# Performance work log

Hardware: AMD Instinct MI355X
Metric: run time of the kernel (lower is better)

The kernel has to match this reference:

```python
import jax, jax.numpy as jnp
import numpy as np

B, N, D, H = 4, 4096, 1024, 16
DH = D // H            # 64
GH = 4 * DH            # gate hidden = 256
FREQ = N // 2 + 1      # 2049
INV_SQRT2 = 0.7071067811865476


def _ln(x, g, b, eps=1e-6):
    mu = jnp.mean(x, axis=-1, keepdims=True)
    var = jnp.mean((x - mu) ** 2, axis=-1, keepdims=True)
    return (x - mu) / jnp.sqrt(var + eps) * g + b


def _xavier(k, out_f, in_f, gain=0.8):
    bound = gain * (6.0 / (in_f + out_f)) ** 0.5
    return jax.random.uniform(k, (out_f, in_f), jnp.float32, -bound, bound)


def setup_inputs() -> dict:
    key = jax.random.key(0)
    ks = jax.random.split(key, 8)
    return {
        'x': jax.random.normal(ks[0], (B, N, D), jnp.float32),
        'Wq': _xavier(ks[1], D, D),
        'Wv': _xavier(ks[2], D, D),
        'Wo': _xavier(ks[3], D, D),
        'ln_g': jnp.ones((DH,), jnp.float32),
        'ln_b': jnp.zeros((DH,), jnp.float32),
        'Wgup': _xavier(ks[4], GH, DH),
        'Wgdn': _xavier(ks[5], 2 * FREQ, GH),
        'Wwup': _xavier(ks[6], GH, DH),
        'Wwdn': _xavier(ks[7], N, GH),
    }


def reference(x, Wq, Wv, Wo, ln_g, ln_b, Wgup, Wgdn, Wwup, Wwdn):
    Bx, Nx, Dx = x.shape
    # projections -> [B, H, N, DH]
    q = (x @ Wq.T).reshape(Bx, Nx, H, DH).transpose(0, 2, 1, 3)
    v = (x @ Wv.T).reshape(Bx, Nx, H, DH).transpose(0, 2, 1, 3)
    # per-head summary token -> complex spectral gate over FREQ bins
    bar = _ln(q.mean(axis=2), ln_g, ln_b)                    # [B, H, DH]
    gr = (jax.nn.silu(bar @ Wgup.T) @ Wgdn.T)               # [B, H, 2*FREQ]
    gr = gr.reshape(Bx, H, FREQ, 2)
    gate = jax.lax.complex(gr[..., 0], gr[..., 1])           # [B, H, FREQ]
    # spectral mixing (chunk == seq_len, power-of-two path)
    spec = jnp.fft.rfft(v, axis=2, norm='ortho') * gate[..., None]
    v_t = jnp.fft.irfft(spec, n=Nx, axis=2, norm='ortho')    # [B, H, N, DH]
    # Haar wavelet refinement
    even, odd = v_t[..., ::2, :], v_t[..., 1::2, :]
    w = jnp.concatenate([even + odd, even - odd], axis=-2) * INV_SQRT2
    s = (jax.nn.silu(bar @ Wwup.T) @ Wwdn.T)[..., None]      # [B, H, N, 1]
    w = w * s
    half = Nx // 2
    low, high = w[..., :half, :], w[..., half:, :]
    # interleave even/odd back along seq dim
    refine = jnp.stack([low + high, low - high], axis=-2).reshape(Bx, H, Nx, DH) * INV_SQRT2
    v_t = v_t + refine
    y = v_t.transpose(0, 2, 1, 3).reshape(Bx, Nx, Dx)
    return y @ Wo.T
```

## Files before the change

kernel.cpp:

```cpp
#include <hip/hip_runtime.h>

constexpr int CB = 4, CN = 4096, CD = 1024, CH = 16, CDH = 64, CGH = 256, CFREQ = 2049, CBH = 64;

constexpr size_t OFF_XSUM = 0;
constexpr size_t OFF_HG   = 4096;
constexpr size_t OFF_HW   = OFF_HG + (size_t)CBH * CGH;
constexpr size_t OFF_GATE = OFF_HW + (size_t)CBH * CGH;
constexpr size_t OFF_S    = OFF_GATE + (size_t)CBH * 2 * CFREQ;
constexpr size_t OFF_CA   = OFF_S + (size_t)CBH * CN;
constexpr size_t OFF_CD   = OFF_CA + (size_t)CBH * (CN / 2);
constexpr size_t OFF_TW   = OFF_CD + (size_t)CBH * (CN / 2);
constexpr size_t OFF_VCOL = OFF_TW + 8192;
constexpr size_t OFF_XHI  = OFF_VCOL + (size_t)CB * CD * CN;
constexpr size_t OFF_XLO  = OFF_XHI + (size_t)CB * CN * CD / 2;
constexpr size_t OFF_WVHI = OFF_XLO + (size_t)CB * CN * CD / 2;
constexpr size_t OFF_WVLO = OFF_WVHI + (size_t)CD * CD / 2;
constexpr size_t OFF_WOHI = OFF_WVLO + (size_t)CD * CD / 2;
constexpr size_t OFF_WOLO = OFF_WOHI + (size_t)CD * CD / 2;

typedef __bf16 bf16x8 __attribute__((ext_vector_type(8)));
typedef __bf16 bf16x4 __attribute__((ext_vector_type(4)));
typedef float  f32x4  __attribute__((ext_vector_type(4)));
typedef float  f32x16 __attribute__((ext_vector_type(16)));

__device__ __forceinline__ float silu_f(float x) { return x / (1.0f + expf(-x)); }

__device__ __forceinline__ void gload16(const void* g, void* l) {
    __builtin_amdgcn_global_load_lds(
        reinterpret_cast<const __attribute__((address_space(1))) unsigned int*>(
            reinterpret_cast<uintptr_t>(g)),
        reinterpret_cast<__attribute__((address_space(3))) unsigned int*>(
            reinterpret_cast<uintptr_t>(l)),
        16, 0, 0);
}

__device__ __forceinline__ float2 cadd(float2 a, float2 b) { return make_float2(a.x + b.x, a.y + b.y); }
__device__ __forceinline__ float2 csub(float2 a, float2 b) { return make_float2(a.x - b.x, a.y - b.y); }
__device__ __forceinline__ float2 cmul(float2 a, float2 b) { return make_float2(a.x * b.x - a.y * b.y, a.x * b.y + a.y * b.x); }
__device__ __forceinline__ float2 cmulc(float2 a, float2 b) { return make_float2(a.x * b.x + a.y * b.y, a.y * b.x - a.x * b.y); }
__device__ __forceinline__ float2 mulni(float2 a) { return make_float2(a.y, -a.x); }
__device__ __forceinline__ float2 mulpi(float2 a) { return make_float2(-a.y, a.x); }

__device__ __forceinline__ int P(int r) { return r + (r >> 3); }

__device__ __forceinline__ int drev8(int k) {
    return ((k & 7) << 9) | (((k >> 3) & 7) << 6) | (((k >> 6) & 7) << 3) | ((k >> 9) & 7);
}

__device__ __forceinline__ void dft8_fwd(const float2 a[8], float2 A[8]) {
    float2 t0 = cadd(a[0], a[4]), t1 = csub(a[0], a[4]);
    float2 t2 = cadd(a[2], a[6]), t3 = mulni(csub(a[2], a[6]));
    float2 t4 = cadd(a[1], a[5]), t5 = csub(a[1], a[5]);
    float2 t6 = cadd(a[3], a[7]), t7 = mulni(csub(a[3], a[7]));
    float2 u0 = cadd(t0, t2), u1 = csub(t0, t2);
    float2 u2 = cadd(t1, t3), u3 = csub(t1, t3);
    float2 u4 = cadd(t4, t6), u5 = mulni(csub(t4, t6));
    float2 u6 = cadd(t5, t7), u7 = csub(t5, t7);
    const float s = 0.70710678118654752f;
    float2 w6 = make_float2(s * (u6.x + u6.y), s * (u6.y - u6.x));
    float2 w7 = make_float2(s * (u7.y - u7.x), -s * (u7.x + u7.y));
    A[0] = cadd(u0, u4); A[4] = csub(u0, u4);
    A[2] = cadd(u1, u5); A[6] = csub(u1, u5);
    A[1] = cadd(u2, w6); A[5] = csub(u2, w6);
    A[3] = cadd(u3, w7); A[7] = csub(u3, w7);
}

__device__ __forceinline__ void dft8_inv(const float2 a[8], float2 A[8]) {
    float2 t0 = cadd(a[0], a[4]), t1 = csub(a[0], a[4]);
    float2 t2 = cadd(a[2], a[6]), t3 = mulpi(csub(a[2], a[6]));
    float2 t4 = cadd(a[1], a[5]), t5 = csub(a[1], a[5]);
    float2 t6 = cadd(a[3], a[7]), t7 = mulpi(csub(a[3], a[7]));
    float2 u0 = cadd(t0, t2), u1 = csub(t0, t2);
    float2 u2 = cadd(t1, t3), u3 = csub(t1, t3);
    float2 u4 = cadd(t4, t6), u5 = mulpi(csub(t4, t6));
    float2 u6 = cadd(t5, t7), u7 = csub(t5, t7);
    const float s = 0.70710678118654752f;
    float2 w6 = make_float2(s * (u6.x - u6.y), s * (u6.x + u6.y));
    float2 w7 = make_float2(-s * (u7.x + u7.y), s * (u7.x - u7.y));
    A[0] = cadd(u0, u4); A[4] = csub(u0, u4);
    A[2] = cadd(u1, u5); A[6] = csub(u1, u5);
    A[1] = cadd(u2, w6); A[5] = csub(u2, w6);
    A[3] = cadd(u3, w7); A[7] = csub(u3, w7);
}

template <int M>
__device__ __forceinline__ void fwd_stage(float2* buf, const float2* __restrict__ tw, int t) {
    int j = t & (M - 1);
    int i0 = ((t & ~(M - 1)) << 3) + j;
    constexpr int TS = 512 / M;
    float2 a[8], A[8];
#pragma unroll
    for (int c = 0; c < 8; ++c) a[c] = buf[P(i0 + c * M)];
    dft8_fwd(a, A);
#pragma unroll
    for (int p = 0; p < 8; ++p) {
        float2 v = (M > 1 && p) ? cmul(A[p], tw[j * p * TS]) : A[p];
        buf[P(i0 + p * M)] = v;
    }
}

template <int M>
__device__ __forceinline__ void inv_stage(float2* buf, const float2* __restrict__ tw, int t) {
    int j = t & (M - 1);
    int i0 = ((t & ~(M - 1)) << 3) + j;
    constexpr int TS = 512 / M;
    float2 a[8], A[8];
#pragma unroll
    for (int c = 0; c < 8; ++c) {
        float2 v = buf[P(i0 + c * M)];
        a[c] = (M > 1 && c) ? cmulc(v, tw[j * c * TS]) : v;
    }
    dft8_inv(a, A);
#pragma unroll
    for (int p = 0; p < 8; ++p) buf[P(i0 + p * M)] = A[p];
}

__global__ void k_tw(float* twf) {
    int i = blockIdx.x * 256 + threadIdx.x;
    if (i < 4096) {
        double ang = -2.0 * 3.14159265358979323846 * (double)i / 4096.0;
        twf[2 * i]     = (float)cos(ang);
        twf[2 * i + 1] = (float)sin(ang);
    }
}

__global__ __launch_bounds__(256) void k_meansplit(const float* __restrict__ X, float* __restrict__ xsum,
                                                   __bf16* __restrict__ hi, __bf16* __restrict__ lo) {
    int b = blockIdx.y;
    int c = blockIdx.x;
    int t = threadIdx.x;
    int half = t >> 7;
    int col = (t & 127) * 8;
    size_t base = (size_t)b * CN * CD + ((size_t)c * 64 + half * 32) * CD + col;
    float acc[8];
#pragma unroll
    for (int j = 0; j < 8; ++j) acc[j] = 0.f;
    for (int n = 0; n < 32; ++n) {
        size_t o = base + (size_t)n * CD;
        float4 v0 = *(const float4*)(X + o);
        float4 v1 = *(const float4*)(X + o + 4);
        float vv[8] = {v0.x, v0.y, v0.z, v0.w, v1.x, v1.y, v1.z, v1.w};
        bf16x8 hv, lv;
#pragma unroll
        for (int j = 0; j < 8; ++j) {
            acc[j] += vv[j];
            __bf16 h = (__bf16)vv[j];
            hv[j] = h;
            lv[j] = (__bf16)(vv[j] - (float)h);
        }
        *(bf16x8*)&hi[o] = hv;
        *(bf16x8*)&lo[o] = lv;
    }
#pragma unroll
    for (int j = 0; j < 8; ++j) atomicAdd(&xsum[b * CD + col + j], acc[j]);
}

__global__ __launch_bounds__(256) void k_barhidden(const float* __restrict__ xsum,
                                                   const float* __restrict__ Wq,
                                                   const float* __restrict__ ln_g,
                                                   const float* __restrict__ ln_b,
                                                   const float* __restrict__ Wgup,
                                                   const float* __restrict__ Wwup,
                                                   float* __restrict__ hg, float* __restrict__ hw) {
    int bh = blockIdx.x;
    int b = bh >> 4, h = bh & 15;
    int t = threadIdx.x;
    __shared__ float part[256];
    __shared__ float bar_s[64];
    int dh = t >> 2, seg = t & 3;
    const float* wrow = Wq + (size_t)(h * 64 + dh) * CD + seg * 256;
    const float* xs = xsum + b * CD + seg * 256;
    float acc = 0.f;
    for (int i = 0; i < 256; i += 4) {
        float4 w4 = *(const float4*)(wrow + i);
        float4 x4 = *(const float4*)(xs + i);
        acc += w4.x * x4.x + w4.y * x4.y + w4.z * x4.z + w4.w * x4.w;
    }
    part[t] = acc;
    __syncthreads();
    if (t < 64) {
        float q = (part[4 * t] + part[4 * t + 1] + part[4 * t + 2] + part[4 * t + 3]) * (1.0f / 4096.0f);
        float mu = q;
        for (int o = 32; o >= 1; o >>= 1) mu += __shfl_xor(mu, o, 64);
        mu *= (1.0f / 64.0f);
        float dev = q - mu;
        float vv = dev * dev;
        for (int o = 32; o >= 1; o >>= 1) vv += __shfl_xor(vv, o, 64);
        vv *= (1.0f / 64.0f);
        bar_s[t] = dev / sqrtf(vv + 1e-6f) * ln_g[t] + ln_b[t];
    }
    __syncthreads();
    const float* gup = Wgup + (size_t)t * CDH;
    const float* wup = Wwup + (size_t)t * CDH;
    float ag = 0.f, aw = 0.f;
    for (int i = 0; i < CDH; i += 4) {
        float4 bb = *(const float4*)(&bar_s[i]);
        float4 g4 = *(const float4*)(gup + i);
        float4 w4 = *(const float4*)(wup + i);
        ag += g4.x * bb.x + g4.y * bb.y + g4.z * bb.z + g4.w * bb.w;
        aw += w4.x * bb.x + w4.y * bb.y + w4.z * bb.z + w4.w * bb.w;
    }
    hg[bh * CGH + t] = silu_f(ag);
    hw[bh * CGH + t] = silu_f(aw);
}

__global__ __launch_bounds__(256) void k_gategemv(const float* __restrict__ Wgdn,
                                                  const float* __restrict__ Wwdn,
                                                  const float* __restrict__ hg,
                                                  const float* __restrict__ hw,
                                                  float* __restrict__ gate, float* __restrict__ sbuf) {
    int z = blockIdx.z;
    const float* Wd = z ? Wwdn : Wgdn;
    const float* hid = z ? hw : hg;
    float* out = z ? sbuf : gate;
    int Kout = z ? CN : 2 * CFREQ;
    int bh0 = blockIdx.y * 8;
    int t = threadIdx.x;
    int k = blockIdx.x * 256 + t;
    __shared__ float Lh[8][256];
    for (int g = 0; g < 8; ++g) Lh[g][t] = hid[(size_t)(bh0 + g) * CGH + t];
    __syncthreads();
    if (k >= Kout) return;
    float accv[8] = {0.f, 0.f, 0.f, 0.f, 0.f, 0.f, 0.f, 0.f};
    const float* wrow = Wd + (size_t)k * CGH;
    for (int j4 = 0; j4 < 64; ++j4) {
        float4 wv = *(const float4*)(wrow + 4 * j4);
#pragma unroll
        for (int g = 0; g < 8; ++g) {
            accv[g] += wv.x * Lh[g][4 * j4] + wv.y * Lh[g][4 * j4 + 1] +
                       wv.z * Lh[g][4 * j4 + 2] + wv.w * Lh[g][4 * j4 + 3];
        }
    }
    for (int g = 0; g < 8; ++g) out[(size_t)(bh0 + g) * Kout + k] = accv[g];
}

__global__ __launch_bounds__(256) void k_coef(const float* __restrict__ sbuf,
                                              float* __restrict__ ca, float* __restrict__ cd) {
    int bh = blockIdx.y;
    int i = blockIdx.x * 256 + threadIdx.x;
    float s0 = sbuf[(size_t)bh * CN + i];
    float s1 = sbuf[(size_t)bh * CN + 2048 + i];
    ca[(size_t)bh * 2048 + i] = 1.0f + 0.5f * (s0 + s1);
    cd[(size_t)bh * 2048 + i] = 0.5f * (s0 - s1);
}

__global__ __launch_bounds__(256) void k_split(const float* __restrict__ src,
                                               __bf16* __restrict__ hi, __bf16* __restrict__ lo,
                                               int n4) {
    int i = blockIdx.x * 256 + threadIdx.x;
    int stride = gridDim.x * 256;
    for (; i < n4; i += stride) {
        float4 v = ((const float4*)src)[i];
        __bf16 h0 = (__bf16)v.x, h1 = (__bf16)v.y, h2 = (__bf16)v.z, h3 = (__bf16)v.w;
        bf16x4 hv = {h0, h1, h2, h3};
        bf16x4 lv = {(__bf16)(v.x - (float)h0), (__bf16)(v.y - (float)h1),
                     (__bf16)(v.z - (float)h2), (__bf16)(v.w - (float)h3)};
        *(bf16x4*)&hi[4 * (size_t)i] = hv;
        *(bf16x4*)&lo[4 * (size_t)i] = lv;
    }
}

__global__ __launch_bounds__(256) void k_tsplit(const float* __restrict__ Vcol,
                                                __bf16* __restrict__ hi, __bf16* __restrict__ lo) {
    __shared__ float tile[32][33];
    int bx = blockIdx.x;
    int by = blockIdx.y;
    int b  = blockIdx.z;
    int t = threadIdx.x;
    int d = t >> 3, n4 = (t & 7) * 4;
    const float* src = Vcol + ((size_t)b * CD + by * 32 + d) * CN + bx * 32 + n4;
    float4 v = *(const float4*)src;
    tile[d][n4] = v.x; tile[d][n4 + 1] = v.y; tile[d][n4 + 2] = v.z; tile[d][n4 + 3] = v.w;
    __syncthreads();
    int n = t >> 3, d4 = (t & 7) * 4;
    size_t o = ((size_t)b * CN + bx * 32 + n) * CD + by * 32 + d4;
    float x0 = tile[d4][n], x1 = tile[d4 + 1][n], x2 = tile[d4 + 2][n], x3 = tile[d4 + 3][n];
    __bf16 h0 = (__bf16)x0, h1 = (__bf16)x1, h2 = (__bf16)x2, h3 = (__bf16)x3;
    bf16x4 hv = {h0, h1, h2, h3};
    bf16x4 lv = {(__bf16)(x0 - (float)h0), (__bf16)(x1 - (float)h1),
                 (__bf16)(x2 - (float)h2), (__bf16)(x3 - (float)h3)};
    *(bf16x4*)&hi[o] = hv;
    *(bf16x4*)&lo[o] = lv;
}

template <int TRANS>
__global__ __launch_bounds__(512, 2) void k_mfma_gemm(const __bf16* __restrict__ Ahi,
                                                      const __bf16* __restrict__ Alo,
                                                      const __bf16* __restrict__ Bhi,
                                                      const __bf16* __restrict__ Blo,
                                                      float* __restrict__ C) {
    __shared__ __align__(16) __bf16 lds[2][4][256 * 32];
    int t = threadIdx.x;
    int l = t & 63, w = t >> 6;
    int wm = w >> 2, wn = w & 3;
    int hw = blockIdx.x;
    int xcd = hw & 7, slot = hw >> 3;
    int m0 = (xcd * 8 + (slot >> 2)) * 256;
    int n0 = (slot & 3) * 256;

    int pl = w >> 1;
    const __bf16* gsrc = (pl == 0) ? Ahi : (pl == 1) ? Alo : (pl == 2) ? Bhi : Blo;
    int gr0 = (pl < 2) ? m0 : n0;
    unsigned o[8];
    int rl0[8];
#pragma unroll
    for (int i = 0; i < 8; ++i) {
        int rl = (w & 1) * 128 + i * 16 + (l >> 2);
        unsigned sq = (unsigned)((l & 3) ^ ((rl >> 2) & 3));
        o[i] = (unsigned)(gr0 + rl) * 1024u + sq * 8u;
        rl0[i] = (w & 1) * 128 + i * 16;
    }

    f32x16 acc[4][2];
#pragma unroll
    for (int mi = 0; mi < 4; ++mi)
#pragma unroll
        for (int ni = 0; ni < 2; ++ni)
#pragma unroll
            for (int q = 0; q < 16; ++q) acc[mi][ni][q] = 0.f;

#pragma unroll
    for (int i = 0; i < 8; ++i)
        gload16(gsrc + (size_t)o[i], &lds[0][pl][rl0[i] * 32]);
    __syncthreads();

#pragma unroll 1
    for (int t32 = 0; t32 < 32; ++t32) {
        int cur = t32 & 1;
        size_t koff = (size_t)(t32 + 1) * 32;
        bool pf = (t32 + 1) < 32;
        bf16x8 bfr[2][2][2];
#pragma unroll
        for (int p = 0; p < 4; ++p) {
            if (pf) {
                gload16(gsrc + ((size_t)o[2 * p] + koff), &lds[cur ^ 1][pl][rl0[2 * p] * 32]);
                gload16(gsrc + ((size_t)o[2 * p + 1] + koff), &lds[cur ^ 1][pl][rl0[2 * p + 1] * 32]);
            }
            bf16x8 afr[2][2];
            int arow = wm * 128 + p * 32 + (l & 31);
            int akey = (arow >> 2) & 3;
#pragma unroll
            for (int s = 0; s < 2; ++s) {
                int sl = ((l >> 5) + 2 * s) ^ akey;
                afr[s][0] = *(const bf16x8*)&lds[cur][0][arow * 32 + sl * 8];
                afr[s][1] = *(const bf16x8*)&lds[cur][1][arow * 32 + sl * 8];
            }
            if (p == 0) {
#pragma unroll
                for (int ni = 0; ni < 2; ++ni) {
                    int bcol = wn * 64 + ni * 32 + (l & 31);
                    int bkey = (bcol >> 2) & 3;
#pragma unroll
                    for (int s = 0; s < 2; ++s) {
                        int sl = ((l >> 5) + 2 * s) ^ bkey;
                        bfr[ni][s][0] = *(const bf16x8*)&lds[cur][2][bcol * 32 + sl * 8];
                        bfr[ni][s][1] = *(const bf16x8*)&lds[cur][3][bcol * 32 + sl * 8];
                    }
                }
            }
            __builtin_amdgcn_s_barrier();
            __builtin_amdgcn_s_setprio(1);
#pragma unroll
            for (int ni = 0; ni < 2; ++ni)
#pragma unroll
                for (int s = 0; s < 2; ++s) {
                    acc[p][ni] = __builtin_amdgcn_mfma_f32_32x32x16_bf16(afr[s][0], bfr[ni][s][0], acc[p][ni], 0, 0, 0);
                    acc[p][ni] = __builtin_amdgcn_mfma_f32_32x32x16_bf16(afr[s][0], bfr[ni][s][1], acc[p][ni], 0, 0, 0);
                    acc[p][ni] = __builtin_amdgcn_mfma_f32_32x32x16_bf16(afr[s][1], bfr[ni][s][0], acc[p][ni], 0, 0, 0);
                }
            __builtin_amdgcn_s_setprio(0);
            __builtin_amdgcn_s_barrier();
        }
        __syncthreads();
    }

    if (TRANS) {
        int b = m0 >> 12;
        int tokb = (m0 & 4095) + wm * 128;
#pragma unroll
        for (int mi = 0; mi < 4; ++mi)
#pragma unroll
            for (int ni = 0; ni < 2; ++ni) {
                int dcol = n0 + wn * 64 + ni * 32 + (l & 31);
                float* base = C + ((size_t)(b * CD + dcol)) * CN;
#pragma unroll
                for (int q = 0; q < 4; ++q) {
                    int tok = tokb + mi * 32 + 8 * q + 4 * (l >> 5);
                    f32x4 v = {acc[mi][ni][4 * q], acc[mi][ni][4 * q + 1],
                               acc[mi][ni][4 * q + 2], acc[mi][ni][4 * q + 3]};
                    *(f32x4*)&base[tok] = v;
                }
            }
    } else {
#pragma unroll
        for (int mi = 0; mi < 4; ++mi)
#pragma unroll
            for (int ni = 0; ni < 2; ++ni) {
                int cc = n0 + wn * 64 + ni * 32 + (l & 31);
#pragma unroll
                for (int q = 0; q < 4; ++q) {
                    int r0 = m0 + wm * 128 + mi * 32 + 8 * q + 4 * (l >> 5);
#pragma unroll
                    for (int j = 0; j < 4; ++j)
                        C[(size_t)(r0 + j) * CD + cc] = acc[mi][ni][4 * q + j];
                }
            }
    }
}

__global__ __launch_bounds__(512) void k_fft(float* __restrict__ Vcol,
                                             const float* __restrict__ gateB,
                                             const float* __restrict__ caB,
                                             const float* __restrict__ cdB,
                                             const float2* __restrict__ tw) {
    __shared__ float2 buf[4608];
    int blk = blockIdx.x;
    int bh = blk >> 5, pr = blk & 31;
    int t = threadIdx.x;
    float* colA = Vcol + (size_t)(bh * 64 + pr * 2) * CN;
    float* colB = colA + CN;

    {
        float2 a[8], A[8];
#pragma unroll
        for (int c = 0; c < 8; ++c) {
            int n = t + 512 * c;
            a[c] = make_float2(colA[n], colB[n]);
        }
        dft8_fwd(a, A);
#pragma unroll
        for (int p = 0; p < 8; ++p) {
            float2 v = p ? cmul(A[p], tw[t * p]) : A[p];
            buf[P(t + 512 * p)] = v;
        }
    }
    __syncthreads();
    fwd_stage<64>(buf, tw, t);  __syncthreads();
    fwd_stage<8>(buf, tw, t);   __syncthreads();
    fwd_stage<1>(buf, tw, t);   __syncthreads();

    {
        const float2* g2 = (const float2*)gateB + (size_t)bh * CFREQ;
        for (int k = t; k <= 2048; k += 512) {
            int r  = drev8(k);
            int r2 = drev8((4096 - k) & 4095);
            float2 Zk = buf[P(r)];
            float2 Zj = buf[P(r2)];
            float2 Av = make_float2(0.5f * (Zk.x + Zj.x), 0.5f * (Zk.y - Zj.y));
            float2 Bv = make_float2(0.5f * (Zk.y + Zj.y), -0.5f * (Zk.x - Zj.x));
            float2 g = g2[k];
            float2 SA = cmul(g, Av);
            float2 SB = cmul(g, Bv);
            buf[P(r)] = make_float2(SA.x - SB.y, SA.y + SB.x);
            if (r2 != r) buf[P(r2)] = make_float2(SA.x + SB.y, SB.x - SA.y);
        }
    }
    __syncthreads();

    inv_stage<1>(buf, tw, t);   __syncthreads();
    inv_stage<8>(buf, tw, t);   __syncthreads();
    inv_stage<64>(buf, tw, t);  __syncthreads();

    {
        float2 a[8], A[8];
#pragma unroll
        for (int c = 0; c < 8; ++c) {
            float2 v = buf[P(t + 512 * c)];
            a[c] = c ? cmulc(v, tw[t * c]) : v;
        }
        dft8_inv(a, A);
        const float scale = 1.0f / 4096.0f;
        const float* ca = caB + (size_t)bh * 2048;
        const float* cd = cdB + (size_t)bh * 2048;
#pragma unroll
        for (int p = 0; p < 8; ++p) {
            int n = t + 512 * p;
            int i = n >> 1;
            float A_ = ca[i] * scale, D_ = cd[i] * scale;
            float ox = __shfl_xor(A[p].x, 1, 64);
            float oy = __shfl_xor(A[p].y, 1, 64);
            colA[n] = A_ * A[p].x + D_ * ox;
            colB[n] = A_ * A[p].y + D_ * oy;
        }
    }
}

extern "C" void kernel_launch(void* const* d_in, const int* in_sizes, int n_in,
                              void* d_out, int out_size, void* d_ws, size_t ws_size,
                              hipStream_t stream) {
    const float* x    = (const float*)d_in[0];
    const float* Wq   = (const float*)d_in[1];
    const float* Wv   = (const float*)d_in[2];
    const float* Wo   = (const float*)d_in[3];
    const float* ln_g = (const float*)d_in[4];
    const float* ln_b = (const float*)d_in[5];
    const float* Wgup = (const float*)d_in[6];
    const float* Wgdn = (const float*)d_in[7];
    const float* Wwup = (const float*)d_in[8];
    const float* Wwdn = (const float*)d_in[9];
    float* ws  = (float*)d_ws;
    float* out = (float*)d_out;

    __bf16* xhi  = (__bf16*)(ws + OFF_XHI);
    __bf16* xlo  = (__bf16*)(ws + OFF_XLO);
    __bf16* wvhi = (__bf16*)(ws + OFF_WVHI);
    __bf16* wvlo = (__bf16*)(ws + OFF_WVLO);
    __bf16* wohi = (__bf16*)(ws + OFF_WOHI);
    __bf16* wolo = (__bf16*)(ws + OFF_WOLO);
    __bf16* v2hi = (__bf16*)(ws + OFF_XHI);
    __bf16* v2lo = (__bf16*)(ws + OFF_XLO);

    hipMemsetAsync(ws + OFF_XSUM, 0, 4096 * sizeof(float), stream);
    k_tw<<<16, 256, 0, stream>>>(ws + OFF_TW);
    k_meansplit<<<dim3(64, 4), 256, 0, stream>>>(x, ws + OFF_XSUM, xhi, xlo);
    k_barhidden<<<64, 256, 0, stream>>>(ws + OFF_XSUM, Wq, ln_g, ln_b, Wgup, Wwup,
                                        ws + OFF_HG, ws + OFF_HW);
    k_gategemv<<<dim3(17, 8, 2), 256, 0, stream>>>(Wgdn, Wwdn, ws + OFF_HG, ws + OFF_HW,
                                                   ws + OFF_GATE, ws + OFF_S);
    k_coef<<<dim3(8, 64), 256, 0, stream>>>(ws + OFF_S, ws + OFF_CA, ws + OFF_CD);

    k_split<<<1024, 256, 0, stream>>>(Wv, wvhi, wvlo, CD * CD / 4);
    k_split<<<1024, 256, 0, stream>>>(Wo, wohi, wolo, CD * CD / 4);

    k_mfma_gemm<1><<<256, 512, 0, stream>>>(xhi, xlo, wvhi, wvlo, ws + OFF_VCOL);

    k_fft<<<2048, 512, 0, stream>>>(ws + OFF_VCOL, ws + OFF_GATE, ws + OFF_CA, ws + OFF_CD,
                                    (const float2*)(ws + OFF_TW));

    k_tsplit<<<dim3(128, 32, 4), 256, 0, stream>>>(ws + OFF_VCOL, v2hi, v2lo);

    k_mfma_gemm<0><<<256, 512, 0, stream>>>(v2hi, v2lo, wohi, wolo, out);
}
```

Measured before the change: 403.3 us.

## Fuse final forward and first inverse FFT stages with a precomputed bit-reversed Hermitian gate

The packed two-column complex FFT now multiplies by a Hermitian-extended gate stored in bit-reversed order. That gate is built once by a new small kernel into the freed Wv-hi workspace. This replaces the last forward radix-8 stage, the real/imag unpacking gate pass and the first inverse stage with one in-register forward-DFT8, gate multiply and inverse-DFT8. It removes two shared-memory round trips and two barriers per FFT block. The cost is an extra launch and a 2MB gate table read, and an occupancy hint is added to launch bounds.

```diff
diff --git a/kernel.cpp b/kernel.cpp
--- a/kernel.cpp
+++ b/kernel.cpp
@@ -122,6 +122,18 @@
         twf[2 * i]     = (float)cos(ang);
         twf[2 * i + 1] = (float)sin(ang);
     }
+}
+
+__global__ __launch_bounds__(256) void k_grev(const float* __restrict__ gateB,
+                                              float2* __restrict__ grev) {
+    int bh = blockIdx.y;
+    int r = blockIdx.x * 256 + threadIdx.x;
+    int k = drev8(r);
+    const float2* g2 = (const float2*)gateB + (size_t)bh * CFREQ;
+    float2 g;
+    if (k <= 2048) g = g2[k];
+    else { float2 gg = g2[4096 - k]; g = make_float2(gg.x, -gg.y); }
+    grev[(size_t)bh * 4096 + r] = g;
 }
 
 __global__ __launch_bounds__(256) void k_meansplit(const float* __restrict__ X, float* __restrict__ xsum,
@@ -408,11 +420,11 @@
     }
 }
 
-__global__ __launch_bounds__(512) void k_fft(float* __restrict__ Vcol,
-                                             const float* __restrict__ gateB,
-                                             const float* __restrict__ caB,
-                                             const float* __restrict__ cdB,
-                                             const float2* __restrict__ tw) {
+__global__ __launch_bounds__(512, 8) void k_fft(float* __restrict__ Vcol,
+                                                const float2* __restrict__ grevB,
+                                                const float* __restrict__ caB,
+                                                const float* __restrict__ cdB,
+                                                const float2* __restrict__ tw) {
     __shared__ float2 buf[4608];
     int blk = blockIdx.x;
     int bh = blk >> 5, pr = blk & 31;
@@ -437,27 +449,22 @@
     __syncthreads();
     fwd_stage<64>(buf, tw, t);  __syncthreads();
     fwd_stage<8>(buf, tw, t);   __syncthreads();
-    fwd_stage<1>(buf, tw, t);   __syncthreads();
 
     {
-        const float2* g2 = (const float2*)gateB + (size_t)bh * CFREQ;
-        for (int k = t; k <= 2048; k += 512) {
-            int r  = drev8(k);
-            int r2 = drev8((4096 - k) & 4095);
-            float2 Zk = buf[P(r)];
-            float2 Zj = buf[P(r2)];
-            float2 Av = make_float2(0.5f * (Zk.x + Zj.x), 0.5f * (Zk.y - Zj.y));
-            float2 Bv = make_float2(0.5f * (Zk.y + Zj.y), -0.5f * (Zk.x - Zj.x));
-            float2 g = g2[k];
-            float2 SA = cmul(g, Av);
-            float2 SB = cmul(g, Bv);
-            buf[P(r)] = make_float2(SA.x - SB.y, SA.y + SB.x);
-            if (r2 != r) buf[P(r2)] = make_float2(SA.x + SB.y, SB.x - SA.y);
-        }
-    }
-    __syncthreads();
-
-    inv_stage<1>(buf, tw, t);   __syncthreads();
+        const float2* gr = grevB + (size_t)bh * 4096 + (t << 3);
+        int i0 = t << 3;
+        float2 a[8], A[8];
+#pragma unroll
+        for (int c = 0; c < 8; ++c) a[c] = buf[P(i0 + c)];
+        dft8_fwd(a, A);
+#pragma unroll
+        for (int p = 0; p < 8; ++p) A[p] = cmul(gr[p], A[p]);
+        dft8_inv(A, a);
+#pragma unroll
+        for (int p = 0; p < 8; ++p) buf[P(i0 + p)] = a[p];
+    }
+    __syncthreads();
+
     inv_stage<8>(buf, tw, t);   __syncthreads();
     inv_stage<64>(buf, tw, t);  __syncthreads();
 
@@ -509,6 +516,7 @@
     __bf16* wolo = (__bf16*)(ws + OFF_WOLO);
     __bf16* v2hi = (__bf16*)(ws + OFF_XHI);
     __bf16* v2lo = (__bf16*)(ws + OFF_XLO);
+    float2* grev = (float2*)(ws + OFF_WVHI);
 
     hipMemsetAsync(ws + OFF_XSUM, 0, 4096 * sizeof(float), stream);
     k_tw<<<16, 256, 0, stream>>>(ws + OFF_TW);
@@ -524,7 +532,9 @@
 
     k_mfma_gemm<1><<<256, 512, 0, stream>>>(xhi, xlo, wvhi, wvlo, ws + OFF_VCOL);
 
-    k_fft<<<2048, 512, 0, stream>>>(ws + OFF_VCOL, ws + OFF_GATE, ws + OFF_CA, ws + OFF_CD,
+    k_grev<<<dim3(16, 64), 256, 0, stream>>>(ws + OFF_GATE, grev);
+
+    k_fft<<<2048, 512, 0, stream>>>(ws + OFF_VCOL, grev, ws + OFF_CA, ws + OFF_CD,
                                     (const float2*)(ws + OFF_TW));
 
     k_tsplit<<<dim3(128, 32, 4), 256, 0, stream>>>(ws + OFF_VCOL, v2hi, v2lo);
```

New measurement: 421.9 us. 1.05x slower.
